# Performance work log

Measured on AMD Instinct MI355X. Metric: run time of the kernel, lower is better.

Reference implementation:

```python
import jax, jax.numpy as jnp
import numpy as np

B, T, D, E = 8, 2048, 256, 4
D_E = D // E


def setup_inputs() -> dict:
    key = jax.random.key(0)
    ks = jax.random.split(key, 12)
    s = 1.0 / np.sqrt(D)
    x = jax.random.normal(ks[0], (B, T, D), dtype=jnp.float32)
    # ensure max(seq_len) == T so the padded input matches this_batch_padlen
    seq_len = jnp.concatenate([
        jax.random.randint(ks[1], (B - 1,), T // 2, T),
        jnp.array([T]),
    ]).astype(jnp.int32)
    return {
        "x": x,
        "seq_len": seq_len,
        "wq": jax.random.uniform(ks[2], (D, D), jnp.float32, -s, s),
        "bq": jax.random.uniform(ks[3], (D,), jnp.float32, -s, s),
        "wk": jax.random.uniform(ks[4], (D, D), jnp.float32, -s, s),
        "bk": jax.random.uniform(ks[5], (D,), jnp.float32, -s, s),
        "wv": jax.random.uniform(ks[6], (D, D), jnp.float32, -s, s),
        "bv": jax.random.uniform(ks[7], (D,), jnp.float32, -s, s),
        "wo": jax.random.uniform(ks[8], (D, D), jnp.float32, -s, s),
        "bo": jax.random.uniform(ks[9], (D,), jnp.float32, -s, s),
        "theta": jnp.array([50.0], dtype=jnp.float32),
    }


def _split_heads(y):
    # faithful to torch: [B,T,D] -> permute(0,2,1) -> [B,D,T] -> reshape(B*E, T, D_E)
    return jnp.transpose(y, (0, 2, 1)).reshape(B * E, T, D_E)


def reference(x, seq_len, wq, bq, wk, bk, wv, bv, wo, bo, theta):
    Q = _split_heads(x @ wq.T + bq)          # [B*E, T, D_E]
    K = _split_heads(x @ wk.T + bk)          # [B*E, T, D_E]
    V = _split_heads(x @ wv.T + bv)          # [B*E, T, D_E]

    # padding mask: zero out query rows (and key cols) past seq_len[i]
    pos = jnp.arange(T)
    valid = (pos[None, :] < seq_len[:, None])                 # [B, T]
    mask_q = jnp.repeat(valid, E, axis=0).astype(Q.dtype)     # [B*E, T]
    Q = Q * mask_q[:, :, None]
    K = K * mask_q[:, :, None]

    scale = jnp.sqrt(jnp.float32(T))
    att = jnp.einsum('bqd,bkd->bqk', Q, K) / scale            # [B*E, T, T]

    # Gaussian positional penalty (is_punish=True)
    tpos = jnp.arange(T, dtype=jnp.float32)
    diff = tpos[None, :] - tpos[:, None]                      # j - i
    punish = jnp.exp(-(diff ** 2) / (theta[0] ** 2))          # [T, T]
    att = att * punish[None, :, :]

    att = jnp.where(att == 0.0, jnp.float32(-2e20), att)
    att = jax.nn.softmax(att, axis=2)

    ctx = jnp.einsum('bqk,bkd->bqd', att, V)                  # [B*E, T, D_E]
    # faithful inverse of _split_heads: permute(0,2,1)->reshape(B,D,T)->permute
    ctx = jnp.transpose(jnp.transpose(ctx, (0, 2, 1)).reshape(B, D, T), (0, 2, 1))
    A = ctx @ wo.T + bo
    return A + x
```

## Files before the change

### kernel.cpp

```cpp
#include <hip/hip_runtime.h>
#include <math.h>
#include <stdint.h>

#define B_SZ   8
#define T_SEQ  2048
#define DIM    256
#define NH     32
#define DE     64
#define BAND   509
#define M_ROWS (B_SZ * T_SEQ)

typedef __attribute__((ext_vector_type(8))) short short8;
typedef __attribute__((ext_vector_type(4))) float floatx4;
typedef unsigned short ushort_t;

__device__ __forceinline__ ushort_t f2bf(float x) {
    unsigned u = __float_as_uint(x);
    u += 0x7fffu + ((u >> 16) & 1u);
    return (ushort_t)(u >> 16);
}
__device__ __forceinline__ float bf2f(ushort_t b) {
    return __uint_as_float(((unsigned)b) << 16);
}
__device__ __forceinline__ unsigned pack2(float a, float b) {
    return (unsigned)f2bf(a) | ((unsigned)f2bf(b) << 16);
}

__device__ __forceinline__ double pd_exact(int d, float th) {
    float df  = (float)d;
    float arg = (-(df * df)) / (th * th);
    double pdd = exp((double)arg);
    if (pdd < 1.17549435082228751e-38)
        return rint(pdd * 0x1p149) * 0x1p-149;
    return (double)(float)pdd;
}

__global__ __launch_bounds__(256) void prep_kernel(
    const float* __restrict__ x,
    const float* __restrict__ wq, const float* __restrict__ wk,
    const float* __restrict__ wv, const float* __restrict__ wo,
    const float* __restrict__ theta,
    ushort_t* __restrict__ xb, ushort_t* __restrict__ wb,
    float* __restrict__ thr_g, float* __restrict__ pdf_g)
{
    const int bid = blockIdx.x, tid = threadIdx.x;
    if (bid < 2048) {
        size_t i8 = ((size_t)bid * 256 + tid) * 8;
        float4 a = *(const float4*)(x + i8);
        float4 b = *(const float4*)(x + i8 + 4);
        uint4 o;
        o.x = pack2(a.x, a.y); o.y = pack2(a.z, a.w);
        o.z = pack2(b.x, b.y); o.w = pack2(b.z, b.w);
        *(uint4*)(xb + i8) = o;
    } else if (bid < 2176) {
        size_t w8 = ((size_t)(bid - 2048) * 256 + tid) * 8;
        int which = (int)(w8 >> 16);
        const float* src = (which == 0) ? wq : (which == 1) ? wk : (which == 2) ? wv : wo;
        size_t off = w8 & 65535;
        float4 a = *(const float4*)(src + off);
        float4 b = *(const float4*)(src + off + 4);
        uint4 o;
        o.x = pack2(a.x, a.y); o.y = pack2(a.z, a.w);
        o.z = pack2(b.x, b.y); o.w = pack2(b.z, b.w);
        *(uint4*)(wb + w8) = o;
    } else {
        int i = (bid - 2176) * 256 + tid;
        float th = theta[0];
        if (i < 384) pdf_g[i] = (float)pd_exact(i, th);
        if (i < 288) {
            double pdv = pd_exact(321 + i, th);
            thr_g[i] = (pdv == 0.0) ? __builtin_inff() : (float)(0x1p-150 / pdv);
        }
    }
}

__global__ __launch_bounds__(256, 2) void proj_qkv_mfma(
    const ushort_t* __restrict__ xb, const ushort_t* __restrict__ wb,
    const float* __restrict__ bq, const float* __restrict__ bk,
    const float* __restrict__ bv, const int* __restrict__ seq_len,
    ushort_t* __restrict__ Qh, ushort_t* __restrict__ Kh, ushort_t* __restrict__ Vh)
{
    __shared__ __align__(16) ushort_t Ls[4][64][68];
    const int wave = threadIdx.x >> 6, lane = threadIdx.x & 63;
    const int quad = lane >> 4, l15 = lane & 15;
    const int task = blockIdx.x * 4 + wave;
    const int nt64 = task % 12;
    const int mstrip = task / 12;
    const int mode = nt64 >> 2;
    const int nloc_base = (nt64 & 3) * 64;
    const ushort_t* Wp = wb + (size_t)mode * 65536;
    const int m0 = mstrip * 64;
    const int bb = m0 >> 11;
    const int th0 = (m0 >> 6) & 31;
    const int sl = seq_len[bb];
    ushort_t* outp = (mode == 0) ? Qh : (mode == 1) ? Kh : Vh;
    const float* bias = (mode == 0) ? bq : (mode == 1) ? bk : bv;
    const int hh = bb * 4 + (nloc_base >> 6);
    const float oscale = (mode == 0) ? 0.022097086912079612f : 1.0f;

    short8 Bf[4][8];
    #pragma unroll
    for (int nt = 0; nt < 4; ++nt) {
        int nrow = nloc_base + nt * 16 + l15;
        #pragma unroll
        for (int ks = 0; ks < 8; ++ks)
            Bf[nt][ks] = *(const short8*)(Wp + (size_t)nrow * 256 + ks * 32 + quad * 8);
    }
    float bias4[4];
    #pragma unroll
    for (int nt = 0; nt < 4; ++nt) bias4[nt] = bias[nloc_base + nt * 16 + l15];

    short8 Acur[8];
    #pragma unroll
    for (int ks = 0; ks < 8; ++ks)
        Acur[ks] = *(const short8*)(xb + (size_t)(m0 + l15) * 256 + ks * 32 + quad * 8);

    #pragma unroll
    for (int mb = 0; mb < 4; ++mb) {
        const int mb0 = m0 + mb * 16;
        short8 Anext[8];
        if (mb < 3) {
            #pragma unroll
            for (int ks = 0; ks < 8; ++ks)
                Anext[ks] = *(const short8*)(xb + (size_t)(mb0 + 16 + l15) * 256 + ks * 32 + quad * 8);
        }
        floatx4 acc[4];
        #pragma unroll
        for (int nt = 0; nt < 4; ++nt) acc[nt] = (floatx4){0.f, 0.f, 0.f, 0.f};
        #pragma unroll
        for (int ks = 0; ks < 8; ++ks)
            #pragma unroll
            for (int nt = 0; nt < 4; ++nt)
                acc[nt] = __builtin_amdgcn_mfma_f32_16x16x32_bf16(Acur[ks], Bf[nt][ks], acc[nt], 0, 0, 0);
        #pragma unroll
        for (int nt = 0; nt < 4; ++nt) {
            float v0 = (acc[nt][0] + bias4[nt]) * oscale;
            float v1 = (acc[nt][1] + bias4[nt]) * oscale;
            float v2 = (acc[nt][2] + bias4[nt]) * oscale;
            float v3 = (acc[nt][3] + bias4[nt]) * oscale;
            uint2 pk; pk.x = pack2(v0, v1); pk.y = pack2(v2, v3);
            *(uint2*)&Ls[wave][nt * 16 + l15][mb * 16 + quad * 4] = pk;
        }
        #pragma unroll
        for (int ks = 0; ks < 8; ++ks) Acur[ks] = Anext[ks];
    }

    #pragma unroll
    for (int s = 0; s < 16; ++s) {
        int dl = s * 4 + quad;
        int e0 = l15 * 4;
        uint2 pk = *(const uint2*)&Ls[wave][dl][e0];
        int q = dl * 32 + th0;
        if (mode <= 1 && q >= sl) { pk.x = 0u; pk.y = 0u; }
        *(uint2*)(outp + (((size_t)hh * T_SEQ + q) << 6) + e0) = pk;
    }
}

__global__ __launch_bounds__(256) void vtrans_kernel(const ushort_t* __restrict__ Vh,
                                                     ushort_t* __restrict__ VTp)
{
    __shared__ ushort_t Vs[256][66];
    const int tid = threadIdx.x;
    const int h = blockIdx.x >> 3, chunk = blockIdx.x & 7;
    const ushort_t* src = Vh + ((size_t)(h * T_SEQ + chunk * 256)) * DE;
    #pragma unroll
    for (int rep = 0; rep < 8; ++rep) {
        int f = rep * 256 + tid;
        int row = f >> 3, c8 = (f & 7) * 8;
        *(uint4*)&Vs[row][c8] = *(const uint4*)(src + (size_t)row * DE + c8);
    }
    __syncthreads();
    const int w = tid >> 6, lane = tid & 63;
    const int half = lane >> 5;
    const int c32 = lane & 31;
    const int cbase = c32 * 8;
    const int blk = cbase >> 6;
    const int cin = cbase & 63;
    #pragma unroll
    for (int rr = 0; rr < 8; ++rr) {
        int e = w * 16 + rr * 2 + half;
        ushort_t tmp[8];
        #pragma unroll
        for (int t = 0; t < 8; ++t) {
            int ci = cin + t;
            int j = blk * 64 + (ci >> 2) + 16 * (ci & 3);
            tmp[t] = Vs[j][e];
        }
        *(uint4*)(VTp + ((size_t)(h * DE + e)) * T_SEQ + chunk * 256 + cbase) = *(uint4*)tmp;
    }
}

__global__ __launch_bounds__(256) void meanv_partial(const ushort_t* __restrict__ Vh,
                                                     float* __restrict__ mv) {
    __shared__ float red[32][72];
    const int blk = blockIdx.x;
    const int h = blk >> 3, chunk = blk & 7;
    const int tid = threadIdx.x;
    const int r0 = tid >> 3;
    const int es = (tid & 7) * 8;
    const ushort_t* p = Vh + ((size_t)h * T_SEQ + chunk * 256 + r0) * DE + es;
    float s[8] = {};
    #pragma unroll
    for (int k = 0; k < 8; ++k) {
        uint4 u = *(const uint4*)(p + (size_t)k * 32 * DE);
        const ushort_t* w = (const ushort_t*)&u;
        #pragma unroll
        for (int i = 0; i < 8; ++i) s[i] += bf2f(w[i]);
    }
    #pragma unroll
    for (int i = 0; i < 8; ++i) red[r0][es + i] = s[i];
    __syncthreads();
    if (tid < 64) {
        float t = 0.f;
        #pragma unroll
        for (int g = 0; g < 32; ++g) t += red[g][tid];
        atomicAdd(&mv[h * DE + tid], t);
    }
}

__global__ __launch_bounds__(256) void attn_mfma_kernel(
    const ushort_t* __restrict__ Qh, const ushort_t* __restrict__ Kh,
    const ushort_t* __restrict__ VTp, const float* __restrict__ thr_g,
    const float* __restrict__ pdf_g, const float* __restrict__ mvs,
    const int* __restrict__ seq_len, ushort_t* __restrict__ ctxb)
{
    __shared__ ushort_t Ks [64][72];
    __shared__ ushort_t VTs[64][72];
    __shared__ ushort_t Ps [4][16][72];
    __shared__ float pdfs[384];
    __shared__ float thrs[288];

    const int tid  = threadIdx.x;
    const int wave = tid >> 6;
    const int lane = tid & 63;
    const int quad = lane >> 4;
    const int l15  = lane & 15;
    const int bid   = blockIdx.x;
    const int inner = bid >> 3;
    const int h  = ((inner >> 5) << 3) | (bid & 7);
    const int q0 = (inner & 31) * 64;
    const int b  = h >> 2;
    const int sl = seq_len[b];
    const float invT = 1.0f / (float)T_SEQ;
    ushort_t* outbase = ctxb + ((size_t)b * T_SEQ + q0) * DIM + (size_t)(h & 3) * 64;

    if (q0 >= sl) {
        #pragma unroll
        for (int nt = 0; nt < 4; ++nt) {
            ushort_t mval = f2bf(mvs[h * DE + l15 + 16 * nt] * invT);
            #pragma unroll
            for (int r = 0; r < 4; ++r)
                outbase[(size_t)(wave * 16 + quad * 4 + r) * DIM + l15 + 16 * nt] = mval;
        }
        return;
    }

    for (int i = tid; i < 384; i += 256) pdfs[i] = pdf_g[i];
    for (int i = tid; i < 288; i += 256) thrs[i] = thr_g[i];

    short8 qa0, qa1;
    {
        const ushort_t* qp = Qh + ((size_t)h * T_SEQ + q0 + wave * 16 + l15) * DE + quad * 8;
        qa0 = *(const short8*)(qp);
        qa1 = *(const short8*)(qp + 32);
    }

    float l_acc[4] = {0.f, 0.f, 0.f, 0.f};
    floatx4 cacc[4];
    #pragma unroll
    for (int nt = 0; nt < 4; ++nt) cacc[nt] = (floatx4){0.f, 0.f, 0.f, 0.f};

    int jlo = q0 - BAND;      if (jlo < 0) jlo = 0;
    int jhi = q0 + 63 + BAND; if (jhi > sl - 1) jhi = sl - 1;
    const int jt0 = jlo >> 6, jt1 = jhi >> 6;

    const int krow = tid >> 3;
    const int kc8  = (tid & 7) * 8;
    const ushort_t* Kbp = Kh + (size_t)h * T_SEQ * DE;
    const ushort_t* Vbp = VTp + (size_t)h * DE * T_SEQ;
    uint4 kpre0, kpre1, vpre0, vpre1;
    {
        const int j0 = jt0 << 6;
        kpre0 = *(const uint4*)(Kbp + (size_t)(j0 + krow) * DE + kc8);
        kpre1 = *(const uint4*)(Kbp + (size_t)(j0 + krow + 32) * DE + kc8);
        vpre0 = *(const uint4*)(Vbp + (size_t)krow * T_SEQ + j0 + kc8);
        vpre1 = *(const uint4*)(Vbp + (size_t)(krow + 32) * T_SEQ + j0 + kc8);
    }

    for (int jt = jt0; jt <= jt1; ++jt) {
        const int j0 = jt << 6;
        __syncthreads();
        *(uint4*)&Ks[krow][kc8]       = kpre0;
        *(uint4*)&Ks[krow + 32][kc8]  = kpre1;
        *(uint4*)&VTs[krow][kc8]      = vpre0;
        *(uint4*)&VTs[krow + 32][kc8] = vpre1;
        __syncthreads();
        if (jt < jt1) {
            const int jn = j0 + 64;
            kpre0 = *(const uint4*)(Kbp + (size_t)(jn + krow) * DE + kc8);
            kpre1 = *(const uint4*)(Kbp + (size_t)(jn + krow + 32) * DE + kc8);
            vpre0 = *(const uint4*)(Vbp + (size_t)krow * T_SEQ + jn + kc8);
            vpre1 = *(const uint4*)(Vbp + (size_t)(krow + 32) * T_SEQ + jn + kc8);
        }

        floatx4 S[4];
        #pragma unroll
        for (int nt = 0; nt < 4; ++nt) {
            short8 kb0 = *(const short8*)&Ks[l15 + 16 * nt][quad * 8];
            short8 kb1 = *(const short8*)&Ks[l15 + 16 * nt][32 + quad * 8];
            floatx4 z = {0.f, 0.f, 0.f, 0.f};
            z = __builtin_amdgcn_mfma_f32_16x16x32_bf16(qa0, kb0, z, 0, 0, 0);
            z = __builtin_amdgcn_mfma_f32_16x16x32_bf16(qa1, kb1, z, 0, 0, 0);
            S[nt] = z;
        }

        const int off = j0 - q0;
        float p[4][4];
        if (off >= -320 && off <= 320) {
            #pragma unroll
            for (int nt = 0; nt < 4; ++nt) {
                int jg = j0 + l15 + 16 * nt;
                bool jv = (jg < sl);
                #pragma unroll
                for (int r = 0; r < 4; ++r) {
                    int dd = jg - (q0 + wave * 16 + quad * 4 + r);
                    dd = dd < 0 ? -dd : dd;
                    float av = S[nt][r] * pdfs[dd];
                    av = jv ? av : -1e30f;
                    p[nt][r] = __expf(av);
                }
            }
        } else {
            #pragma unroll
            for (int nt = 0; nt < 4; ++nt) {
                int jg = j0 + l15 + 16 * nt;
                #pragma unroll
                for (int r = 0; r < 4; ++r) {
                    int dd = jg - (q0 + wave * 16 + quad * 4 + r);
                    dd = dd < 0 ? -dd : dd;
                    p[nt][r] = (fabsf(S[nt][r]) > thrs[dd - 321]) ? 1.0f : 0.0f;
                }
            }
        }

        #pragma unroll
        for (int r = 0; r < 4; ++r) {
            l_acc[r] += (p[0][r] + p[1][r]) + (p[2][r] + p[3][r]);
            uint2 pk;
            pk.x = pack2(p[0][r], p[1][r]);
            pk.y = pack2(p[2][r], p[3][r]);
            *(uint2*)&Ps[wave][quad * 4 + r][l15 * 4] = pk;
        }
        short8 pa0 = *(const short8*)&Ps[wave][l15][quad * 8];
        short8 pa1 = *(const short8*)&Ps[wave][l15][32 + quad * 8];
        #pragma unroll
        for (int nt = 0; nt < 4; ++nt) {
            short8 vb0 = *(const short8*)&VTs[l15 + 16 * nt][quad * 8];
            short8 vb1 = *(const short8*)&VTs[l15 + 16 * nt][32 + quad * 8];
            floatx4 c = cacc[nt];
            c = __builtin_amdgcn_mfma_f32_16x16x32_bf16(pa0, vb0, c, 0, 0, 0);
            c = __builtin_amdgcn_mfma_f32_16x16x32_bf16(pa1, vb1, c, 0, 0, 0);
            cacc[nt] = c;
        }
    }

    #pragma unroll
    for (int r = 0; r < 4; ++r) {
        float lv = l_acc[r];
        #pragma unroll
        for (int o = 1; o <= 8; o <<= 1) lv += __shfl_xor(lv, o);
        l_acc[r] = 1.0f / lv;
    }
    #pragma unroll
    for (int nt = 0; nt < 4; ++nt) {
        #pragma unroll
        for (int r = 0; r < 4; ++r) {
            int row = wave * 16 + quad * 4 + r;
            int qg = q0 + row;
            float o = cacc[nt][r] * l_acc[r];
            if (qg >= sl) o = mvs[h * DE + l15 + 16 * nt] * invT;
            outbase[(size_t)row * DIM + l15 + 16 * nt] = f2bf(o);
        }
    }
}

__global__ __launch_bounds__(256, 2) void proj_o_mfma(
    const ushort_t* __restrict__ ctx, const ushort_t* __restrict__ wb,
    const float* __restrict__ bo, const float* __restrict__ x,
    float* __restrict__ out)
{
    __shared__ __align__(16) ushort_t As[32][264];
    const int tid = threadIdx.x;
    const int wave = tid >> 6, lane = tid & 63;
    const int quad = lane >> 4, l15 = lane & 15;
    const int m0 = blockIdx.x * 32;
    const int n0 = wave * 64;
    const ushort_t* Wp = wb + (size_t)3 * 65536;

    #pragma unroll
    for (int rep = 0; rep < 4; ++rep) {
        int f = rep * 256 + tid;
        int row = f >> 5, c8 = (f & 31) * 8;
        *(uint4*)&As[row][c8] = *(const uint4*)(ctx + (size_t)(m0 + row) * 256 + c8);
    }

    short8 Bf[4][8];
    #pragma unroll
    for (int nt = 0; nt < 4; ++nt) {
        int nrow = n0 + nt * 16 + l15;
        #pragma unroll
        for (int ks = 0; ks < 8; ++ks)
            Bf[nt][ks] = *(const short8*)(Wp + (size_t)nrow * 256 + ks * 32 + quad * 8);
    }
    float bias4[4];
    #pragma unroll
    for (int nt = 0; nt < 4; ++nt) bias4[nt] = bo[n0 + nt * 16 + l15];

    __syncthreads();

    #pragma unroll
    for (int mb = 0; mb < 2; ++mb) {
        short8 Af[8];
        #pragma unroll
        for (int ks = 0; ks < 8; ++ks)
            Af[ks] = *(const short8*)&As[mb * 16 + l15][ks * 32 + quad * 8];
        floatx4 acc[4];
        #pragma unroll
        for (int nt = 0; nt < 4; ++nt) acc[nt] = (floatx4){0.f, 0.f, 0.f, 0.f};
        #pragma unroll
        for (int ks = 0; ks < 8; ++ks)
            #pragma unroll
            for (int nt = 0; nt < 4; ++nt)
                acc[nt] = __builtin_amdgcn_mfma_f32_16x16x32_bf16(Af[ks], Bf[nt][ks], acc[nt], 0, 0, 0);
        #pragma unroll
        for (int nt = 0; nt < 4; ++nt) {
            int d = n0 + nt * 16 + l15;
            #pragma unroll
            for (int r = 0; r < 4; ++r) {
                size_t mi = (size_t)(m0 + mb * 16 + quad * 4 + r) * 256 + d;
                out[mi] = acc[nt][r] + bias4[nt] + x[mi];
            }
        }
    }
}

extern "C" void kernel_launch(void* const* d_in, const int* in_sizes, int n_in,
                              void* d_out, int out_size, void* d_ws, size_t ws_size,
                              hipStream_t stream)
{
    (void)in_sizes; (void)n_in; (void)out_size; (void)ws_size;
    const float* x  = (const float*)d_in[0];
    const int*   sl = (const int*)d_in[1];
    const float* wq = (const float*)d_in[2];
    const float* bq = (const float*)d_in[3];
    const float* wk = (const float*)d_in[4];
    const float* bk = (const float*)d_in[5];
    const float* wv = (const float*)d_in[6];
    const float* bv = (const float*)d_in[7];
    const float* wo = (const float*)d_in[8];
    const float* bo = (const float*)d_in[9];
    const float* th = (const float*)d_in[10];
    float* out = (float*)d_out;

    char* ws = (char*)d_ws;
    const size_t SZH = (size_t)M_ROWS * DIM * sizeof(ushort_t);
    ushort_t* xb  = (ushort_t*)(ws);
    ushort_t* wb  = (ushort_t*)(ws + SZH);
    ushort_t* Qh  = (ushort_t*)(ws + SZH + 524288);
    ushort_t* Kh  = (ushort_t*)(ws + 2*SZH + 524288);
    ushort_t* Vh  = (ushort_t*)(ws + 3*SZH + 524288);
    ushort_t* VTp = (ushort_t*)(ws + 4*SZH + 524288);
    ushort_t* Cb  = (ushort_t*)(ws + 5*SZH + 524288);
    float*    Mv  = (float*)   (ws + 6*SZH + 524288);
    float*    Thr = (float*)   (ws + 6*SZH + 524288 + 8192);
    float*    Pdf = (float*)   (ws + 6*SZH + 524288 + 12288);

    hipMemsetAsync(Mv, 0, NH * DE * sizeof(float), stream);
    prep_kernel<<<dim3(2178), dim3(256), 0, stream>>>(x, wq, wk, wv, wo, th, xb, wb, Thr, Pdf);
    proj_qkv_mfma<<<dim3(768), dim3(256), 0, stream>>>(xb, wb, bq, bk, bv, sl, Qh, Kh, Vh);
    vtrans_kernel<<<dim3(NH * 8), dim3(256), 0, stream>>>(Vh, VTp);
    meanv_partial<<<dim3(256), dim3(256), 0, stream>>>(Vh, Mv);
    attn_mfma_kernel<<<dim3(1024), dim3(256), 0, stream>>>(Qh, Kh, VTp, Thr, Pdf, Mv, sl, Cb);
    proj_o_mfma<<<dim3(512), dim3(256), 0, stream>>>(Cb, wb, bo, x, out);
}
```

Measured before the change: 179.3 us.

## Compute transposed scores to feed P directly into MFMA without LDS round-trip

Swaps the MFMA operands so each lane holds scores for one query row across keys, which lets the probabilities be packed in registers as the A operand of the PV MFMA instead of staged through a shared-memory buffer. The V transpose permutation is changed to match the new key ordering within the packed operand. The row-sum reduction becomes a cross-quad shuffle, and the tail mask is split so full tiles skip per-element bounds checks. Block-to-strip mapping is also rotated per head group to spread work. This removes LDS writes/reads and a dependency per tile, at the cost of tighter coupling between the V layout and the MFMA register layout.

```diff
diff --git a/kernel.cpp b/kernel.cpp
--- a/kernel.cpp
+++ b/kernel.cpp
@@ -12,6 +12,7 @@
 
 typedef __attribute__((ext_vector_type(8))) short short8;
 typedef __attribute__((ext_vector_type(4))) float floatx4;
+typedef __attribute__((ext_vector_type(4))) unsigned uintx4;
 typedef unsigned short ushort_t;
 
 __device__ __forceinline__ ushort_t f2bf(float x) {
@@ -183,7 +184,8 @@
         #pragma unroll
         for (int t = 0; t < 8; ++t) {
             int ci = cin + t;
-            int j = blk * 64 + (ci >> 2) + 16 * (ci & 3);
+            int j = blk * 64 + 32 * (ci >> 5) + 4 * ((ci >> 3) & 3)
+                  + 16 * ((ci >> 2) & 1) + (ci & 3);
             tmp[t] = Vs[j][e];
         }
         *(uint4*)(VTp + ((size_t)(h * DE + e)) * T_SEQ + chunk * 256 + cbase) = *(uint4*)tmp;
@@ -226,7 +228,6 @@
 {
     __shared__ ushort_t Ks [64][72];
     __shared__ ushort_t VTs[64][72];
-    __shared__ ushort_t Ps [4][16][72];
     __shared__ float pdfs[384];
     __shared__ float thrs[288];
 
@@ -237,8 +238,10 @@
     const int l15  = lane & 15;
     const int bid   = blockIdx.x;
     const int inner = bid >> 3;
-    const int h  = ((inner >> 5) << 3) | (bid & 7);
-    const int q0 = (inner & 31) * 64;
+    const int g     = inner >> 5;
+    const int strip = ((inner & 31) + g * 8) & 31;
+    const int h  = (g << 3) | (bid & 7);
+    const int q0 = strip * 64;
     const int b  = h >> 2;
     const int sl = seq_len[b];
     const float invT = 1.0f / (float)T_SEQ;
@@ -265,7 +268,7 @@
         qa1 = *(const short8*)(qp + 32);
     }
 
-    float l_acc[4] = {0.f, 0.f, 0.f, 0.f};
+    float l_acc = 0.f;
     floatx4 cacc[4];
     #pragma unroll
     for (int nt = 0; nt < 4; ++nt) cacc[nt] = (floatx4){0.f, 0.f, 0.f, 0.f};
@@ -286,6 +289,8 @@
         vpre0 = *(const uint4*)(Vbp + (size_t)krow * T_SEQ + j0 + kc8);
         vpre1 = *(const uint4*)(Vbp + (size_t)(krow + 32) * T_SEQ + j0 + kc8);
     }
+
+    const int qrow = q0 + wave * 16 + l15;
 
     for (int jt = jt0; jt <= jt1; ++jt) {
         const int j0 = jt << 6;
@@ -303,56 +308,61 @@
             vpre1 = *(const uint4*)(Vbp + (size_t)(krow + 32) * T_SEQ + jn + kc8);
         }
 
-        floatx4 S[4];
+        floatx4 ST[4];
         #pragma unroll
         for (int nt = 0; nt < 4; ++nt) {
-            short8 kb0 = *(const short8*)&Ks[l15 + 16 * nt][quad * 8];
-            short8 kb1 = *(const short8*)&Ks[l15 + 16 * nt][32 + quad * 8];
+            short8 ka0 = *(const short8*)&Ks[l15 + 16 * nt][quad * 8];
+            short8 ka1 = *(const short8*)&Ks[l15 + 16 * nt][32 + quad * 8];
             floatx4 z = {0.f, 0.f, 0.f, 0.f};
-            z = __builtin_amdgcn_mfma_f32_16x16x32_bf16(qa0, kb0, z, 0, 0, 0);
-            z = __builtin_amdgcn_mfma_f32_16x16x32_bf16(qa1, kb1, z, 0, 0, 0);
-            S[nt] = z;
+            z = __builtin_amdgcn_mfma_f32_16x16x32_bf16(ka0, qa0, z, 0, 0, 0);
+            z = __builtin_amdgcn_mfma_f32_16x16x32_bf16(ka1, qa1, z, 0, 0, 0);
+            ST[nt] = z;
         }
 
         const int off = j0 - q0;
+        const int db  = j0 + quad * 4 - qrow;
         float p[4][4];
         if (off >= -320 && off <= 320) {
-            #pragma unroll
-            for (int nt = 0; nt < 4; ++nt) {
-                int jg = j0 + l15 + 16 * nt;
-                bool jv = (jg < sl);
+            if (j0 + 63 < sl) {
+                #pragma unroll
+                for (int nt = 0; nt < 4; ++nt)
+                    #pragma unroll
+                    for (int r = 0; r < 4; ++r) {
+                        int dd = db + nt * 16 + r; dd = dd < 0 ? -dd : dd;
+                        p[nt][r] = __expf(ST[nt][r] * pdfs[dd]);
+                    }
+            } else {
+                #pragma unroll
+                for (int nt = 0; nt < 4; ++nt)
+                    #pragma unroll
+                    for (int r = 0; r < 4; ++r) {
+                        int dd = db + nt * 16 + r; dd = dd < 0 ? -dd : dd;
+                        float v = __expf(ST[nt][r] * pdfs[dd]);
+                        p[nt][r] = (j0 + nt * 16 + quad * 4 + r < sl) ? v : 0.f;
+                    }
+            }
+        } else {
+            #pragma unroll
+            for (int nt = 0; nt < 4; ++nt)
                 #pragma unroll
                 for (int r = 0; r < 4; ++r) {
-                    int dd = jg - (q0 + wave * 16 + quad * 4 + r);
-                    dd = dd < 0 ? -dd : dd;
-                    float av = S[nt][r] * pdfs[dd];
-                    av = jv ? av : -1e30f;
-                    p[nt][r] = __expf(av);
+                    int dd = db + nt * 16 + r; dd = dd < 0 ? -dd : dd;
+                    p[nt][r] = (fabsf(ST[nt][r]) > thrs[dd - 321]) ? 1.0f : 0.0f;
                 }
-            }
-        } else {
-            #pragma unroll
-            for (int nt = 0; nt < 4; ++nt) {
-                int jg = j0 + l15 + 16 * nt;
-                #pragma unroll
-                for (int r = 0; r < 4; ++r) {
-                    int dd = jg - (q0 + wave * 16 + quad * 4 + r);
-                    dd = dd < 0 ? -dd : dd;
-                    p[nt][r] = (fabsf(S[nt][r]) > thrs[dd - 321]) ? 1.0f : 0.0f;
-                }
-            }
-        }
-
-        #pragma unroll
-        for (int r = 0; r < 4; ++r) {
-            l_acc[r] += (p[0][r] + p[1][r]) + (p[2][r] + p[3][r]);
-            uint2 pk;
-            pk.x = pack2(p[0][r], p[1][r]);
-            pk.y = pack2(p[2][r], p[3][r]);
-            *(uint2*)&Ps[wave][quad * 4 + r][l15 * 4] = pk;
-        }
-        short8 pa0 = *(const short8*)&Ps[wave][l15][quad * 8];
-        short8 pa1 = *(const short8*)&Ps[wave][l15][32 + quad * 8];
+        }
+
+        #pragma unroll
+        for (int nt = 0; nt < 4; ++nt)
+            l_acc += (p[nt][0] + p[nt][1]) + (p[nt][2] + p[nt][3]);
+
+        uintx4 t0, t1;
+        t0.x = pack2(p[0][0], p[0][1]); t0.y = pack2(p[0][2], p[0][3]);
+        t0.z = pack2(p[1][0], p[1][1]); t0.w = pack2(p[1][2], p[1][3]);
+        t1.x = pack2(p[2][0], p[2][1]); t1.y = pack2(p[2][2], p[2][3]);
+        t1.z = pack2(p[3][0], p[3][1]); t1.w = pack2(p[3][2], p[3][3]);
+        short8 pa0 = __builtin_bit_cast(short8, t0);
+        short8 pa1 = __builtin_bit_cast(short8, t1);
+
         #pragma unroll
         for (int nt = 0; nt < 4; ++nt) {
             short8 vb0 = *(const short8*)&VTs[l15 + 16 * nt][quad * 8];
@@ -364,20 +374,20 @@
         }
     }
 
-    #pragma unroll
-    for (int r = 0; r < 4; ++r) {
-        float lv = l_acc[r];
-        #pragma unroll
-        for (int o = 1; o <= 8; o <<= 1) lv += __shfl_xor(lv, o);
-        l_acc[r] = 1.0f / lv;
-    }
+    l_acc += __shfl_xor(l_acc, 16);
+    l_acc += __shfl_xor(l_acc, 32);
+    const float linv = 1.0f / l_acc;
+    float linv4[4];
+    #pragma unroll
+    for (int r = 0; r < 4; ++r) linv4[r] = __shfl(linv, quad * 4 + r);
+
     #pragma unroll
     for (int nt = 0; nt < 4; ++nt) {
         #pragma unroll
         for (int r = 0; r < 4; ++r) {
             int row = wave * 16 + quad * 4 + r;
             int qg = q0 + row;
-            float o = cacc[nt][r] * l_acc[r];
+            float o = cacc[nt][r] * linv4[r];
             if (qg >= sl) o = mvs[h * DE + l15 + 16 * nt] * invT;
             outbase[(size_t)row * DIM + l15 + 16 * nt] = f2bf(o);
         }
```

Measured after the change: 182.1 us. Within noise of the previous version (+1.6%).
